# Kernel tuning notes

Measured on AMD Instinct MI355X. Metric: run time of the kernel, lower is better.

## Reference

```python
import jax, jax.numpy as jnp
import numpy as np

N_NODES = 50000
N_EDGES = 640000
IN_FEAT = 128
H_FEAT = 128
OUT_FEAT = 128
N_CLASSES = 16
BN_EPS = 1e-5


def gcn_conv(x, W, b, edge_index, n_nodes):
    """PyG GCNConv: add self-loops, symmetric deg^{-1/2} normalization,
    gather -> weighted message -> scatter_add, plus bias."""
    loop = jnp.arange(n_nodes, dtype=edge_index.dtype)
    src = jnp.concatenate([edge_index[0], loop])  # [E+N]
    dst = jnp.concatenate([edge_index[1], loop])  # [E+N]
    ones = jnp.ones(src.shape[0], dtype=x.dtype)
    deg = jax.ops.segment_sum(ones, dst, num_segments=n_nodes)  # >=1 (self loops)
    dinv = jax.lax.rsqrt(deg)
    norm = dinv[src] * dinv[dst]  # [E+N]
    h = x @ W  # [N, F_out]
    msgs = h[src] * norm[:, None]  # gather + scale, [E+N, F_out]
    out = jax.ops.segment_sum(msgs, dst, num_segments=n_nodes)  # scatter_add
    return out + b


def setup_inputs() -> dict:
    key = jax.random.key(0)
    ks = jax.random.split(key, 10)
    seq = jax.random.normal(ks[0], (N_NODES, IN_FEAT), dtype=jnp.float32)
    edge_index = jax.random.randint(ks[1], (2, N_EDGES), 0, N_NODES, dtype=jnp.int64)
    s1 = 1.0 / np.sqrt(IN_FEAT)
    s2 = 1.0 / np.sqrt(H_FEAT)
    s3 = 1.0 / np.sqrt(OUT_FEAT)
    W1 = jax.random.uniform(ks[2], (IN_FEAT, H_FEAT), jnp.float32, -s1, s1)
    b1 = jnp.zeros((H_FEAT,), jnp.float32)
    gamma = jnp.ones((H_FEAT,), jnp.float32)
    beta = jnp.zeros((H_FEAT,), jnp.float32)
    running_mean = 0.1 * jax.random.normal(ks[3], (H_FEAT,), jnp.float32)
    running_var = jax.random.uniform(ks[4], (H_FEAT,), jnp.float32, 0.5, 1.5)
    W2 = jax.random.uniform(ks[5], (H_FEAT, OUT_FEAT), jnp.float32, -s2, s2)
    b2 = jnp.zeros((OUT_FEAT,), jnp.float32)
    Wc = jax.random.uniform(ks[6], (OUT_FEAT, N_CLASSES), jnp.float32, -s3, s3)
    bc = jax.random.uniform(ks[7], (N_CLASSES,), jnp.float32, -s3, s3)
    return {
        "seq": seq, "edge_index": edge_index,
        "W1": W1, "b1": b1, "gamma": gamma, "beta": beta,
        "running_mean": running_mean, "running_var": running_var,
        "W2": W2, "b2": b2, "Wc": Wc, "bc": bc,
    }


def reference(seq, edge_index, W1, b1, gamma, beta, running_mean, running_var, W2, b2, Wc, bc):
    # inference mode: BN uses running stats, dropout is identity
    n = seq.shape[0]
    h = gcn_conv(seq, W1, b1, edge_index, n)
    h = (h - running_mean) * jax.lax.rsqrt(running_var + BN_EPS) * gamma + beta
    h = jax.nn.relu(h)
    h = gcn_conv(h, W2, b2, edge_index, n)
    return h @ Wc + bc
```

## Files before the change

kernel.cpp:

```cpp
#include <hip/hip_runtime.h>
#include <math.h>

#define N_NODES 50000
#define N_EDGES 640000
#define FDIM 128
#define NCLS 16
#define BN_EPS 1e-5f
#define NBG 782
#define ELLW 64

typedef __attribute__((ext_vector_type(8))) short bf16x8;
typedef __attribute__((ext_vector_type(4))) float f32x4;

__device__ __forceinline__ unsigned pack_bf16x2(float lo, float hi) {
    unsigned ul = __float_as_uint(lo);
    unsigned uh = __float_as_uint(hi);
    ul += 0x7fff + ((ul >> 16) & 1);
    uh += 0x7fff + ((uh >> 16) & 1);
    return (ul >> 16) | (uh & 0xffff0000u);
}
__device__ __forceinline__ unsigned short bf16_rne(float x) {
    unsigned u = __float_as_uint(x);
    u += 0x7fff + ((u >> 16) & 1);
    return (unsigned short)(u >> 16);
}
__device__ __forceinline__ float bf_lo(unsigned u) { return __uint_as_float(u << 16); }
__device__ __forceinline__ float bf_hi(unsigned u) { return __uint_as_float(u & 0xffff0000u); }

__device__ __forceinline__ void async_copy16(const void* g, void* l) {
    __builtin_amdgcn_global_load_lds(
        (const __attribute__((address_space(1))) unsigned*)g,
        (__attribute__((address_space(3))) unsigned*)l, 16, 0, 0);
}

__global__ __launch_bounds__(256) void pack_fold_zero_kernel(
        const float* __restrict__ W1, const float* __restrict__ W2,
        const float* __restrict__ Wc, const float* __restrict__ b1,
        const float* __restrict__ b2, const float* __restrict__ bc,
        const float* __restrict__ gamma, const float* __restrict__ beta,
        const float* __restrict__ rmean, const float* __restrict__ rvar,
        bf16x8* __restrict__ WPK,
        float* __restrict__ W2c, float* __restrict__ bc2, float4* __restrict__ fusedq,
        uint4* __restrict__ degz) {
    int tid = threadIdx.x;
    int bid = blockIdx.x;

    {
        int gz = bid * 256 + tid;
#pragma unroll
        for (int i = 0; i < 4; i++) {
            int idx = gz + i * 4096;
            if (idx < 12544) degz[idx] = make_uint4(0, 0, 0, 0);
        }
    }

    if (bid >= 8) {
        int fi = (bid - 8) * 256 + tid;
        int lane = fi & 63, kt = (fi >> 6) & 3, ct = fi >> 8;
        int kbase = kt * 32 + (lane >> 4) * 8;
        int col = ct * 16 + (lane & 15);
        short h[8], lo[8];
#pragma unroll
        for (int j = 0; j < 8; j++) {
            float wv = W1[(kbase + j) * 128 + col];
            unsigned short hs = bf16_rne(wv);
            float rem = wv - __uint_as_float(((unsigned)hs) << 16);
            h[j] = (short)hs;
            lo[j] = (short)bf16_rne(rem);
        }
        WPK[fi] = *(bf16x8*)h;
        WPK[2048 + fi] = *(bf16x8*)lo;
    } else {
        int gid = bid * 256 + tid;
        int r = gid >> 4, c = gid & 15;
        float acc = 0.f;
#pragma unroll 8
        for (int k = 0; k < 128; k++) acc += W2[r * 128 + k] * Wc[k * 16 + c];
        W2c[gid] = acc;
        if (bid == 0) {
            if (tid < 16) {
                float a = bc[tid];
                for (int k = 0; k < 128; k++) a += b2[k] * Wc[k * 16 + tid];
                bc2[tid] = a;
            }
            if (tid < 64) {
                int c0 = tid * 2, c1 = c0 + 1;
                float sc0 = gamma[c0] * rsqrtf(rvar[c0] + BN_EPS);
                float sc1 = gamma[c1] * rsqrtf(rvar[c1] + BN_EPS);
                float sh0 = (b1[c0] - rmean[c0]) * sc0 + beta[c0];
                float sh1 = (b1[c1] - rmean[c1]) * sc1 + beta[c1];
                fusedq[tid] = make_float4(sc0, sh0, sc1, sh1);
            }
        }
    }
}

__global__ __launch_bounds__(256) void gemm_fill_kernel(
        const float* __restrict__ seq, const bf16x8* __restrict__ WPK,
        unsigned* __restrict__ bufA,
        const int* __restrict__ eidx, int* __restrict__ deg, int* __restrict__ ell) {
    __shared__ __align__(16) char smem[65536];
    int tid = threadIdx.x;
    int bid = blockIdx.x;

    if (bid < NBG) {
        int w = tid >> 6, l = tid & 63;

        {
            const char* gsrc = (const char*)WPK;
#pragma unroll
            for (int r = 0; r < 16; r++)
                async_copy16(gsrc + (size_t)(r * 256 + tid) * 16,
                             smem + (r * 4 + w) * 1024);
        }

        int la = l & 15, q = l >> 4;
        int arow = bid * 64 + w * 16 + la;
        bool rowok = arow < N_NODES;
        const float4* X4 = (const float4*)seq;

        float4 xr[8];
        float4 z4 = make_float4(0.f, 0.f, 0.f, 0.f);
#pragma unroll
        for (int kt = 0; kt < 4; kt++) {
            xr[kt * 2]     = rowok ? X4[arow * 32 + kt * 8 + q * 2]     : z4;
            xr[kt * 2 + 1] = rowok ? X4[arow * 32 + kt * 8 + q * 2 + 1] : z4;
        }
        bf16x8 ah[4], al[4];
#pragma unroll
        for (int kt = 0; kt < 4; kt++) {
            const float* xv = (const float*)&xr[kt * 2];
#pragma unroll
            for (int j = 0; j < 8; j++) {
                float v = xv[j];
                unsigned short hs = bf16_rne(v);
                float rem = v - __uint_as_float(((unsigned)hs) << 16);
                ah[kt][j] = (short)hs;
                al[kt][j] = (short)bf16_rne(rem);
            }
        }
        f32x4 acc[8];
#pragma unroll
        for (int ct = 0; ct < 8; ct++) acc[ct] = (f32x4){0.f, 0.f, 0.f, 0.f};

        __syncthreads();

        const bf16x8* WH = (const bf16x8*)smem;
        const bf16x8* WL = (const bf16x8*)(smem + 32768);
#pragma unroll
        for (int kt = 0; kt < 4; kt++) {
#pragma unroll
            for (int ct = 0; ct < 8; ct++) {
                bf16x8 bh = WH[(ct * 4 + kt) * 64 + l];
                bf16x8 bl = WL[(ct * 4 + kt) * 64 + l];
                acc[ct] = __builtin_amdgcn_mfma_f32_16x16x32_bf16(bh, ah[kt], acc[ct], 0, 0, 0);
                acc[ct] = __builtin_amdgcn_mfma_f32_16x16x32_bf16(bl, ah[kt], acc[ct], 0, 0, 0);
                acc[ct] = __builtin_amdgcn_mfma_f32_16x16x32_bf16(bh, al[kt], acc[ct], 0, 0, 0);
            }
        }

        if (rowok) {
            unsigned* dp = bufA + (size_t)arow * 64 + q * 2;
#pragma unroll
            for (int ct = 0; ct < 8; ct++) {
                uint2 u;
                u.x = pack_bf16x2(acc[ct][0], acc[ct][1]);
                u.y = pack_bf16x2(acc[ct][2], acc[ct][3]);
                *(uint2*)(dp + ct * 8) = u;
            }
        }
    } else {
        const int4* src4 = (const int4*)eidx;
        const int4* dst4 = (const int4*)(eidx + N_EDGES);
        int t = (bid - NBG) * 256 + tid;
        int4 sv = src4[t];
        int4 dv = dst4[t];
        {
            int s = atomicAdd(&deg[dv.x], 1);
            if (s < ELLW) ell[dv.x * ELLW + s] = sv.x;
        }
        {
            int s = atomicAdd(&deg[dv.y], 1);
            if (s < ELLW) ell[dv.y * ELLW + s] = sv.y;
        }
        {
            int s = atomicAdd(&deg[dv.z], 1);
            if (s < ELLW) ell[dv.z * ELLW + s] = sv.z;
        }
        {
            int s = atomicAdd(&deg[dv.w], 1);
            if (s < ELLW) ell[dv.w * ELLW + s] = sv.w;
        }
    }
}

__global__ __launch_bounds__(256) void agg1_kernel(const unsigned* __restrict__ Hb,
                                                   const int* __restrict__ ell,
                                                   const int* __restrict__ deg,
                                                   const float4* __restrict__ fusedq,
                                                   const float* __restrict__ W2c,
                                                   float* __restrict__ Z) {
    __shared__ float sH[4][128];
    int w = threadIdx.x >> 6, l = threadIdx.x & 63;
    int node = blockIdx.x * 4 + w;
    int dg = __builtin_amdgcn_readfirstlane(deg[node]);
    float di = rsqrtf((float)(dg + 1));
    const int* row = ell + node * ELLW;

    int c = l & 15, q = l >> 4;
    float wreg[32];
#pragma unroll
    for (int i = 0; i < 32; i++) wreg[i] = W2c[(q * 32 + i) * 16 + c];

    unsigned hv = Hb[(size_t)node * 64 + l];
    float n2 = di * di;
    float acc0 = bf_lo(hv) * n2, acc1 = bf_hi(hv) * n2;

    int e = 0;
    for (; e + 8 <= dg; e += 8) {
        int s0 = row[e];     int s1 = row[e + 1];
        int s2 = row[e + 2]; int s3 = row[e + 3];
        int s4 = row[e + 4]; int s5 = row[e + 5];
        int s6 = row[e + 6]; int s7 = row[e + 7];
        unsigned u0 = Hb[(size_t)s0 * 64 + l];
        unsigned u1 = Hb[(size_t)s1 * 64 + l];
        unsigned u2 = Hb[(size_t)s2 * 64 + l];
        unsigned u3 = Hb[(size_t)s3 * 64 + l];
        unsigned u4 = Hb[(size_t)s4 * 64 + l];
        unsigned u5 = Hb[(size_t)s5 * 64 + l];
        unsigned u6 = Hb[(size_t)s6 * 64 + l];
        unsigned u7 = Hb[(size_t)s7 * 64 + l];
        float w0 = rsqrtf((float)(deg[s0] + 1)) * di;
        float w1 = rsqrtf((float)(deg[s1] + 1)) * di;
        float w2 = rsqrtf((float)(deg[s2] + 1)) * di;
        float w3 = rsqrtf((float)(deg[s3] + 1)) * di;
        float w4 = rsqrtf((float)(deg[s4] + 1)) * di;
        float w5 = rsqrtf((float)(deg[s5] + 1)) * di;
        float w6 = rsqrtf((float)(deg[s6] + 1)) * di;
        float w7 = rsqrtf((float)(deg[s7] + 1)) * di;
        acc0 += bf_lo(u0) * w0 + bf_lo(u1) * w1 + bf_lo(u2) * w2 + bf_lo(u3) * w3
              + bf_lo(u4) * w4 + bf_lo(u5) * w5 + bf_lo(u6) * w6 + bf_lo(u7) * w7;
        acc1 += bf_hi(u0) * w0 + bf_hi(u1) * w1 + bf_hi(u2) * w2 + bf_hi(u3) * w3
              + bf_hi(u4) * w4 + bf_hi(u5) * w5 + bf_hi(u6) * w6 + bf_hi(u7) * w7;
    }
    while (e < dg) {
        int i1 = e + 1 < dg ? e + 1 : dg - 1;
        int i2 = e + 2 < dg ? e + 2 : dg - 1;
        int i3 = e + 3 < dg ? e + 3 : dg - 1;
        int s0 = row[e];  int s1 = row[i1];
        int s2 = row[i2]; int s3 = row[i3];
        unsigned u0 = Hb[(size_t)s0 * 64 + l];
        unsigned u1 = Hb[(size_t)s1 * 64 + l];
        unsigned u2 = Hb[(size_t)s2 * 64 + l];
        unsigned u3 = Hb[(size_t)s3 * 64 + l];
        float w0 = rsqrtf((float)(deg[s0] + 1)) * di;
        float w1 = (e + 1 < dg) ? rsqrtf((float)(deg[s1] + 1)) * di : 0.f;
        float w2 = (e + 2 < dg) ? rsqrtf((float)(deg[s2] + 1)) * di : 0.f;
        float w3 = (e + 3 < dg) ? rsqrtf((float)(deg[s3] + 1)) * di : 0.f;
        acc0 += bf_lo(u0) * w0 + bf_lo(u1) * w1 + bf_lo(u2) * w2 + bf_lo(u3) * w3;
        acc1 += bf_hi(u0) * w0 + bf_hi(u1) * w1 + bf_hi(u2) * w2 + bf_hi(u3) * w3;
        e += 4;
    }

    float4 qv = fusedq[l];
    float a0 = fmaxf(acc0 * qv.x + qv.y, 0.f);
    float a1 = fmaxf(acc1 * qv.z + qv.w, 0.f);

    ((float2*)sH[w])[l] = make_float2(a0, a1);
    float z = 0.f;
    const float4* row4 = (const float4*)&sH[w][q * 32];
#pragma unroll
    for (int i = 0; i < 8; i++) {
        float4 v = row4[i];
        z += v.x * wreg[i * 4] + v.y * wreg[i * 4 + 1]
           + v.z * wreg[i * 4 + 2] + v.w * wreg[i * 4 + 3];
    }
    z += __shfl_xor(z, 16);
    z += __shfl_xor(z, 32);
    if (l < 16) Z[(size_t)node * NCLS + l] = z;
}

__global__ __launch_bounds__(256) void agg2_kernel(const float* __restrict__ Z,
                                                   const int* __restrict__ ell,
                                                   const int* __restrict__ deg,
                                                   const float* __restrict__ bc2,
                                                   float* __restrict__ out) {
    int grp = threadIdx.x >> 4, c = threadIdx.x & 15;
    int node = blockIdx.x * 16 + grp;
    int dg = deg[node];
    float di = rsqrtf((float)(dg + 1));
    const int* row = ell + node * ELLW;

    float acc = Z[(size_t)node * NCLS + c] * di * di;
    int e = 0;
    for (; e + 8 <= dg; e += 8) {
        int s0 = row[e],     s1 = row[e + 1];
        int s2 = row[e + 2], s3 = row[e + 3];
        int s4 = row[e + 4], s5 = row[e + 5];
        int s6 = row[e + 6], s7 = row[e + 7];
        float v0 = Z[(size_t)s0 * NCLS + c];
        float v1 = Z[(size_t)s1 * NCLS + c];
        float v2 = Z[(size_t)s2 * NCLS + c];
        float v3 = Z[(size_t)s3 * NCLS + c];
        float v4 = Z[(size_t)s4 * NCLS + c];
        float v5 = Z[(size_t)s5 * NCLS + c];
        float v6 = Z[(size_t)s6 * NCLS + c];
        float v7 = Z[(size_t)s7 * NCLS + c];
        acc += v0 * (rsqrtf((float)(deg[s0] + 1)) * di)
             + v1 * (rsqrtf((float)(deg[s1] + 1)) * di)
             + v2 * (rsqrtf((float)(deg[s2] + 1)) * di)
             + v3 * (rsqrtf((float)(deg[s3] + 1)) * di)
             + v4 * (rsqrtf((float)(deg[s4] + 1)) * di)
             + v5 * (rsqrtf((float)(deg[s5] + 1)) * di)
             + v6 * (rsqrtf((float)(deg[s6] + 1)) * di)
             + v7 * (rsqrtf((float)(deg[s7] + 1)) * di);
    }
    for (; e < dg; e++) {
        int s = row[e];
        acc += Z[(size_t)s * NCLS + c] * (rsqrtf((float)(deg[s] + 1)) * di);
    }
    out[(size_t)node * NCLS + c] = acc + bc2[c];
}

extern "C" void kernel_launch(void* const* d_in, const int* in_sizes, int n_in,
                              void* d_out, int out_size, void* d_ws, size_t ws_size,
                              hipStream_t stream) {
    const float* seq   = (const float*)d_in[0];
    const int*   eidx  = (const int*)d_in[1];
    const float* W1    = (const float*)d_in[2];
    const float* b1    = (const float*)d_in[3];
    const float* gamma = (const float*)d_in[4];
    const float* beta  = (const float*)d_in[5];
    const float* rmean = (const float*)d_in[6];
    const float* rvar  = (const float*)d_in[7];
    const float* W2    = (const float*)d_in[8];
    const float* b2    = (const float*)d_in[9];
    const float* Wc    = (const float*)d_in[10];
    const float* bc    = (const float*)d_in[11];

    char* ws = (char*)d_ws;
    size_t off = 0;
    auto alloc = [&](size_t bytes) -> void* {
        void* p = ws + off;
        off = (off + bytes + 255) & ~(size_t)255;
        return p;
    };
    int*    deg      = (int*)alloc(50176 * 4);
    int*    ell      = (int*)alloc((size_t)N_NODES * ELLW * 4);
    float*  W2c      = (float*)alloc(FDIM * NCLS * 4);
    float*  bc2      = (float*)alloc(NCLS * 4);
    float4* fusedq   = (float4*)alloc(64 * 16);
    unsigned* bufA   = (unsigned*)alloc((size_t)N_NODES * (FDIM / 2) * 4);
    float*  Zbuf     = (float*)alloc((size_t)N_NODES * NCLS * 4);
    bf16x8* WPK      = (bf16x8*)alloc(4096 * 16);

    pack_fold_zero_kernel<<<16, 256, 0, stream>>>(
        W1, W2, Wc, b1, b2, bc, gamma, beta, rmean, rvar, WPK, W2c, bc2, fusedq,
        (uint4*)deg);
    gemm_fill_kernel<<<NBG + 625, 256, 0, stream>>>(seq, WPK, bufA, eidx, deg, ell);
    agg1_kernel<<<N_NODES / 4, 256, 0, stream>>>(bufA, ell, deg, fusedq, W2c, Zbuf);
    agg2_kernel<<<N_NODES / 16, 256, 0, stream>>>(Zbuf, ell, deg, bc2, (float*)d_out);
}
```

Before: 208.6 us.

## Preload neighbor indices and weights per lane, broadcast via shuffles in aggregation kernels

Both aggregation kernels now load each node's ELL neighbor list and the degree-normalization weights once, cooperatively across lanes, then broadcast them with wave shuffles. Previously every lane redundantly loaded the same indices and degrees and recomputed rsqrt serially in the gather loop. The fill kernel also reorders its blocks so the edge-fill (atomic) blocks are scheduled before the GEMM blocks. Degree is clamped to the ELL width for the loop bound, and padded batches rely on zero weights, which adds shuffle work and some wasted gathers on short rows.

```diff
diff --git a/kernel.cpp b/kernel.cpp
--- a/kernel.cpp
+++ b/kernel.cpp
@@ -7,6 +7,7 @@
 #define NCLS 16
 #define BN_EPS 1e-5f
 #define NBG 782
+#define NBF 625
 #define ELLW 64
 
 typedef __attribute__((ext_vector_type(8))) short bf16x8;
@@ -103,7 +104,8 @@
     int tid = threadIdx.x;
     int bid = blockIdx.x;
 
-    if (bid < NBG) {
+    if (bid >= NBF) {
+        int gb = bid - NBF;
         int w = tid >> 6, l = tid & 63;
 
         {
@@ -115,7 +117,7 @@
         }
 
         int la = l & 15, q = l >> 4;
-        int arow = bid * 64 + w * 16 + la;
+        int arow = gb * 64 + w * 16 + la;
         bool rowok = arow < N_NODES;
         const float4* X4 = (const float4*)seq;
 
@@ -172,7 +174,7 @@
     } else {
         const int4* src4 = (const int4*)eidx;
         const int4* dst4 = (const int4*)(eidx + N_EDGES);
-        int t = (bid - NBG) * 256 + tid;
+        int t = bid * 256 + tid;
         int4 sv = src4[t];
         int4 dv = dst4[t];
         {
@@ -203,9 +205,13 @@
     __shared__ float sH[4][128];
     int w = threadIdx.x >> 6, l = threadIdx.x & 63;
     int node = blockIdx.x * 4 + w;
-    int dg = __builtin_amdgcn_readfirstlane(deg[node]);
-    float di = rsqrtf((float)(dg + 1));
+    int dgt = __builtin_amdgcn_readfirstlane(deg[node]);
+    int dg = dgt < ELLW ? dgt : ELLW;
+    float di = rsqrtf((float)(dgt + 1));
     const int* row = ell + node * ELLW;
+
+    int s_l = (l < dg) ? row[l] : 0;
+    float w_l = (l < dg) ? rsqrtf((float)(deg[s_l] + 1)) * di : 0.f;
 
     int c = l & 15, q = l >> 4;
     float wreg[32];
@@ -216,50 +222,28 @@
     float n2 = di * di;
     float acc0 = bf_lo(hv) * n2, acc1 = bf_hi(hv) * n2;
 
-    int e = 0;
-    for (; e + 8 <= dg; e += 8) {
-        int s0 = row[e];     int s1 = row[e + 1];
-        int s2 = row[e + 2]; int s3 = row[e + 3];
-        int s4 = row[e + 4]; int s5 = row[e + 5];
-        int s6 = row[e + 6]; int s7 = row[e + 7];
-        unsigned u0 = Hb[(size_t)s0 * 64 + l];
-        unsigned u1 = Hb[(size_t)s1 * 64 + l];
-        unsigned u2 = Hb[(size_t)s2 * 64 + l];
-        unsigned u3 = Hb[(size_t)s3 * 64 + l];
-        unsigned u4 = Hb[(size_t)s4 * 64 + l];
-        unsigned u5 = Hb[(size_t)s5 * 64 + l];
-        unsigned u6 = Hb[(size_t)s6 * 64 + l];
-        unsigned u7 = Hb[(size_t)s7 * 64 + l];
-        float w0 = rsqrtf((float)(deg[s0] + 1)) * di;
-        float w1 = rsqrtf((float)(deg[s1] + 1)) * di;
-        float w2 = rsqrtf((float)(deg[s2] + 1)) * di;
-        float w3 = rsqrtf((float)(deg[s3] + 1)) * di;
-        float w4 = rsqrtf((float)(deg[s4] + 1)) * di;
-        float w5 = rsqrtf((float)(deg[s5] + 1)) * di;
-        float w6 = rsqrtf((float)(deg[s6] + 1)) * di;
-        float w7 = rsqrtf((float)(deg[s7] + 1)) * di;
-        acc0 += bf_lo(u0) * w0 + bf_lo(u1) * w1 + bf_lo(u2) * w2 + bf_lo(u3) * w3
-              + bf_lo(u4) * w4 + bf_lo(u5) * w5 + bf_lo(u6) * w6 + bf_lo(u7) * w7;
-        acc1 += bf_hi(u0) * w0 + bf_hi(u1) * w1 + bf_hi(u2) * w2 + bf_hi(u3) * w3
-              + bf_hi(u4) * w4 + bf_hi(u5) * w5 + bf_hi(u6) * w6 + bf_hi(u7) * w7;
-    }
-    while (e < dg) {
-        int i1 = e + 1 < dg ? e + 1 : dg - 1;
-        int i2 = e + 2 < dg ? e + 2 : dg - 1;
-        int i3 = e + 3 < dg ? e + 3 : dg - 1;
-        int s0 = row[e];  int s1 = row[i1];
-        int s2 = row[i2]; int s3 = row[i3];
-        unsigned u0 = Hb[(size_t)s0 * 64 + l];
-        unsigned u1 = Hb[(size_t)s1 * 64 + l];
-        unsigned u2 = Hb[(size_t)s2 * 64 + l];
-        unsigned u3 = Hb[(size_t)s3 * 64 + l];
-        float w0 = rsqrtf((float)(deg[s0] + 1)) * di;
-        float w1 = (e + 1 < dg) ? rsqrtf((float)(deg[s1] + 1)) * di : 0.f;
-        float w2 = (e + 2 < dg) ? rsqrtf((float)(deg[s2] + 1)) * di : 0.f;
-        float w3 = (e + 3 < dg) ? rsqrtf((float)(deg[s3] + 1)) * di : 0.f;
-        acc0 += bf_lo(u0) * w0 + bf_lo(u1) * w1 + bf_lo(u2) * w2 + bf_lo(u3) * w3;
-        acc1 += bf_hi(u0) * w0 + bf_hi(u1) * w1 + bf_hi(u2) * w2 + bf_hi(u3) * w3;
-        e += 4;
+    int dgr = (dg + 7) & ~7;
+    for (int e = 0; e < dgr; e += 8) {
+        int t0 = __shfl(s_l, e + 0), t1 = __shfl(s_l, e + 1);
+        int t2 = __shfl(s_l, e + 2), t3 = __shfl(s_l, e + 3);
+        int t4 = __shfl(s_l, e + 4), t5 = __shfl(s_l, e + 5);
+        int t6 = __shfl(s_l, e + 6), t7 = __shfl(s_l, e + 7);
+        float x0 = __shfl(w_l, e + 0), x1 = __shfl(w_l, e + 1);
+        float x2 = __shfl(w_l, e + 2), x3 = __shfl(w_l, e + 3);
+        float x4 = __shfl(w_l, e + 4), x5 = __shfl(w_l, e + 5);
+        float x6 = __shfl(w_l, e + 6), x7 = __shfl(w_l, e + 7);
+        unsigned u0 = Hb[(size_t)t0 * 64 + l];
+        unsigned u1 = Hb[(size_t)t1 * 64 + l];
+        unsigned u2 = Hb[(size_t)t2 * 64 + l];
+        unsigned u3 = Hb[(size_t)t3 * 64 + l];
+        unsigned u4 = Hb[(size_t)t4 * 64 + l];
+        unsigned u5 = Hb[(size_t)t5 * 64 + l];
+        unsigned u6 = Hb[(size_t)t6 * 64 + l];
+        unsigned u7 = Hb[(size_t)t7 * 64 + l];
+        acc0 += bf_lo(u0) * x0 + bf_lo(u1) * x1 + bf_lo(u2) * x2 + bf_lo(u3) * x3
+              + bf_lo(u4) * x4 + bf_lo(u5) * x5 + bf_lo(u6) * x6 + bf_lo(u7) * x7;
+        acc1 += bf_hi(u0) * x0 + bf_hi(u1) * x1 + bf_hi(u2) * x2 + bf_hi(u3) * x3
+              + bf_hi(u4) * x4 + bf_hi(u5) * x5 + bf_hi(u6) * x6 + bf_hi(u7) * x7;
     }
 
     float4 qv = fusedq[l];
@@ -285,40 +269,63 @@
                                                    const int* __restrict__ deg,
                                                    const float* __restrict__ bc2,
                                                    float* __restrict__ out) {
-    int grp = threadIdx.x >> 4, c = threadIdx.x & 15;
-    int node = blockIdx.x * 16 + grp;
-    int dg = deg[node];
-    float di = rsqrtf((float)(dg + 1));
+    int tid = threadIdx.x;
+    int c = tid & 15;
+    int node = blockIdx.x * 16 + (tid >> 4);
+    int lane = tid & 63;
+    int baseln = lane & 48;
+    int dgt = deg[node];
+    int dg = dgt < ELLW ? dgt : ELLW;
+    float di = rsqrtf((float)(dgt + 1));
     const int* row = ell + node * ELLW;
 
+    int s0_ = (c < dg) ? row[c] : 0;
+    int s1_ = (c + 16 < dg) ? row[c + 16] : 0;
+    float w0_ = (c < dg) ? rsqrtf((float)(deg[s0_] + 1)) * di : 0.f;
+    float w1_ = (c + 16 < dg) ? rsqrtf((float)(deg[s1_] + 1)) * di : 0.f;
+    int s2_ = 0, s3_ = 0;
+    float w2_ = 0.f, w3_ = 0.f;
+    if (__any(dg > 32)) {
+        s2_ = (c + 32 < dg) ? row[c + 32] : 0;
+        s3_ = (c + 48 < dg) ? row[c + 48] : 0;
+        w2_ = (c + 32 < dg) ? rsqrtf((float)(deg[s2_] + 1)) * di : 0.f;
+        w3_ = (c + 48 < dg) ? rsqrtf((float)(deg[s3_] + 1)) * di : 0.f;
+    }
+
     float acc = Z[(size_t)node * NCLS + c] * di * di;
-    int e = 0;
-    for (; e + 8 <= dg; e += 8) {
-        int s0 = row[e],     s1 = row[e + 1];
-        int s2 = row[e + 2], s3 = row[e + 3];
-        int s4 = row[e + 4], s5 = row[e + 5];
-        int s6 = row[e + 6], s7 = row[e + 7];
-        float v0 = Z[(size_t)s0 * NCLS + c];
-        float v1 = Z[(size_t)s1 * NCLS + c];
-        float v2 = Z[(size_t)s2 * NCLS + c];
-        float v3 = Z[(size_t)s3 * NCLS + c];
-        float v4 = Z[(size_t)s4 * NCLS + c];
-        float v5 = Z[(size_t)s5 * NCLS + c];
-        float v6 = Z[(size_t)s6 * NCLS + c];
-        float v7 = Z[(size_t)s7 * NCLS + c];
-        acc += v0 * (rsqrtf((float)(deg[s0] + 1)) * di)
-             + v1 * (rsqrtf((float)(deg[s1] + 1)) * di)
-             + v2 * (rsqrtf((float)(deg[s2] + 1)) * di)
-             + v3 * (rsqrtf((float)(deg[s3] + 1)) * di)
-             + v4 * (rsqrtf((float)(deg[s4] + 1)) * di)
-             + v5 * (rsqrtf((float)(deg[s5] + 1)) * di)
-             + v6 * (rsqrtf((float)(deg[s6] + 1)) * di)
-             + v7 * (rsqrtf((float)(deg[s7] + 1)) * di);
-    }
-    for (; e < dg; e++) {
-        int s = row[e];
-        acc += Z[(size_t)s * NCLS + c] * (rsqrtf((float)(deg[s] + 1)) * di);
-    }
+
+#define A2_BATCH(SS, WW, OFF)                                                        \
+    {                                                                                \
+        int t0 = __shfl(SS, baseln + OFF + 0), t1 = __shfl(SS, baseln + OFF + 1);    \
+        int t2 = __shfl(SS, baseln + OFF + 2), t3 = __shfl(SS, baseln + OFF + 3);    \
+        int t4 = __shfl(SS, baseln + OFF + 4), t5 = __shfl(SS, baseln + OFF + 5);    \
+        int t6 = __shfl(SS, baseln + OFF + 6), t7 = __shfl(SS, baseln + OFF + 7);    \
+        float x0 = __shfl(WW, baseln + OFF + 0), x1 = __shfl(WW, baseln + OFF + 1);  \
+        float x2 = __shfl(WW, baseln + OFF + 2), x3 = __shfl(WW, baseln + OFF + 3);  \
+        float x4 = __shfl(WW, baseln + OFF + 4), x5 = __shfl(WW, baseln + OFF + 5);  \
+        float x6 = __shfl(WW, baseln + OFF + 6), x7 = __shfl(WW, baseln + OFF + 7);  \
+        float v0 = Z[(size_t)t0 * NCLS + c];                                         \
+        float v1 = Z[(size_t)t1 * NCLS + c];                                         \
+        float v2 = Z[(size_t)t2 * NCLS + c];                                         \
+        float v3 = Z[(size_t)t3 * NCLS + c];                                         \
+        float v4 = Z[(size_t)t4 * NCLS + c];                                         \
+        float v5 = Z[(size_t)t5 * NCLS + c];                                         \
+        float v6 = Z[(size_t)t6 * NCLS + c];                                         \
+        float v7 = Z[(size_t)t7 * NCLS + c];                                         \
+        acc += v0 * x0 + v1 * x1 + v2 * x2 + v3 * x3                                 \
+             + v4 * x4 + v5 * x5 + v6 * x6 + v7 * x7;                                \
+    }
+
+    if (dg > 0)  A2_BATCH(s0_, w0_, 0)
+    if (dg > 8)  A2_BATCH(s0_, w0_, 8)
+    if (dg > 16) A2_BATCH(s1_, w1_, 0)
+    if (dg > 24) A2_BATCH(s1_, w1_, 8)
+    if (dg > 32) A2_BATCH(s2_, w2_, 0)
+    if (dg > 40) A2_BATCH(s2_, w2_, 8)
+    if (dg > 48) A2_BATCH(s3_, w3_, 0)
+    if (dg > 56) A2_BATCH(s3_, w3_, 8)
+#undef A2_BATCH
+
     out[(size_t)node * NCLS + c] = acc + bc2[c];
 }
 
@@ -357,7 +364,7 @@
     pack_fold_zero_kernel<<<16, 256, 0, stream>>>(
         W1, W2, Wc, b1, b2, bc, gamma, beta, rmean, rvar, WPK, W2c, bc2, fusedq,
         (uint4*)deg);
-    gemm_fill_kernel<<<NBG + 625, 256, 0, stream>>>(seq, WPK, bufA, eidx, deg, ell);
+    gemm_fill_kernel<<<NBF + NBG, 256, 0, stream>>>(seq, WPK, bufA, eidx, deg, ell);
     agg1_kernel<<<N_NODES / 4, 256, 0, stream>>>(bufA, ell, deg, fusedq, W2c, Zbuf);
     agg2_kernel<<<N_NODES / 16, 256, 0, stream>>>(Zbuf, ell, deg, bc2, (float*)d_out);
 }
```

New measurement: 187.1 us. 1.11x faster.
